# Optimization experiments

Hardware: AMD Instinct MI355X
Metric: run time of the kernel (lower is better)

The kernel has to match this reference:

```python
import jax, jax.numpy as jnp
import numpy as np


def setup_inputs() -> dict:
    key = jax.random.key(0)
    k1, k2 = jax.random.split(key)
    B, S, D, E = 4, 8192, 1024, 64
    x = jax.random.normal(k1, (B, S, D), dtype=jnp.float32)
    W = jax.random.normal(k2, (E, D), dtype=jnp.float32) * (1.0 / np.sqrt(D))
    return {"x": x, "W": W, "top_k": 1}


EXPERT_CAPACITY = 640


def reference(x, W, top_k):
    # Router logits: small-dim linear (bias=False), jitter=0 so no noise.
    logits = jnp.einsum("bsd,ed->bse", x, W)              # [B,S,E]
    probs = jax.nn.softmax(logits, axis=-1)               # [B,S,E]
    num_experts = W.shape[0]
    # top-k over experts (top_k == 1 here)
    top_k_values, top_k_indices = jax.lax.top_k(probs, top_k)  # [B,S,k]
    # one-hot over experts, summed over the k slots -> [B,S,E] int mask
    expert_indices = jax.nn.one_hot(top_k_indices, num_experts, dtype=jnp.int32).sum(axis=-2)
    # token priority: running count of tokens assigned to each expert along seq
    token_priority = jnp.cumsum(expert_indices, axis=-2)  # [B,S,E]
    capacity_mask = token_priority <= EXPERT_CAPACITY
    expert_indices = expert_indices * capacity_mask.astype(jnp.int32)
    # top_k_values [B,S,1] broadcasts over E (valid only for k==1, as in torch)
    router_probs = top_k_values * expert_indices.astype(top_k_values.dtype)
    return expert_indices, router_probs, logits
```

## Files before the change

kernel.cpp:

```cpp
#include <hip/hip_runtime.h>
#include <hip/hip_bf16.h>

#define NB 4
#define NS 8192
#define ND 1024
#define NE 64
#define NM (NB * NS)
#define CAPACITY 640

#define BM 32
#define BK 64
#define NKT (ND / BK)
#define NBLK (NM / BM)
#define C32PB (NS / BM)

#define OCH 64
#define NOB (NM / OCH)

typedef short short8 __attribute__((ext_vector_type(8)));
typedef unsigned short ushort8 __attribute__((ext_vector_type(8)));
typedef float f32x4 __attribute__((ext_vector_type(4)));

__device__ __forceinline__ int swz(int row, int colshorts) {
    return row * 64 + (colshorts ^ ((row & 7) << 3));
}

__global__ __launch_bounds__(256) void w_conv(const float* __restrict__ W,
                                              unsigned short* __restrict__ Wh,
                                              unsigned short* __restrict__ Wl)
{
    const int i = (blockIdx.x * 256 + threadIdx.x) * 4;
    float4 v = *(const float4*)(W + i);
    float f[4] = {v.x, v.y, v.z, v.w};
    ushort4 h, l;
    unsigned short* hp = &h.x;
    unsigned short* lp = &l.x;
#pragma unroll
    for (int c = 0; c < 4; ++c) {
        __hip_bfloat16 hb = __float2bfloat16(f[c]);
        float r = f[c] - __bfloat162float(hb);
        __hip_bfloat16 lb = __float2bfloat16(r);
        hp[c] = __builtin_bit_cast(unsigned short, hb);
        lp[c] = __builtin_bit_cast(unsigned short, lb);
    }
    *(ushort4*)(Wh + i) = h;
    *(ushort4*)(Wl + i) = l;
}

__global__ __launch_bounds__(128) void k1_mfma(const float* __restrict__ x,
                                               const unsigned short* __restrict__ Wh,
                                               const unsigned short* __restrict__ Wl,
                                               float* __restrict__ logits,
                                               int* __restrict__ idx_ws,
                                               float* __restrict__ prob_ws,
                                               int* __restrict__ hist)
{
    __shared__ char sbuf[8192];
    __shared__ short whs[64 * 64];
    __shared__ short wls[64 * 64];
    __shared__ int lh[NE];

    short* xs_h = (short*)sbuf;
    short* xs_l = (short*)(sbuf + 4096);
    float* sLog = (float*)sbuf;

    const int tid = threadIdx.x;
    const int lane = tid & 63;
    const int wv = tid >> 6;
    const int lr = lane & 15;
    const int kq = lane >> 4;
    const int tok0 = blockIdx.x * BM;

    if (tid < NE) lh[tid] = 0;

    const int xrow = tid >> 2;
    const int xcol = (tid & 3) * 16;
    const float* xsrc = x + (size_t)(tok0 + xrow) * ND + xcol;

    const int we0 = tid >> 3;
    const int wcol = (tid & 7) * 8;

    f32x4 acc[4];
#pragma unroll
    for (int j = 0; j < 4; ++j) acc[j] = (f32x4){0.f, 0.f, 0.f, 0.f};

    float4 px[4], px2[4];
#pragma unroll
    for (int c = 0; c < 4; ++c) px[c] = *(const float4*)(xsrc + c * 4);

    for (int kt = 0; kt < NKT; ++kt) {
        const int k0 = kt * BK;
        if (kt > 0) __syncthreads();

#pragma unroll
        for (int i = 0; i < 4; ++i) {
            const int e = we0 + i * 16;
            const size_t gs = (size_t)e * ND + k0 + wcol;
            ushort8 vh = *(const ushort8*)(Wh + gs);
            ushort8 vl = *(const ushort8*)(Wl + gs);
            *(ushort8*)&whs[swz(e, wcol)] = vh;
            *(ushort8*)&wls[swz(e, wcol)] = vl;
        }

#pragma unroll
        for (int c = 0; c < 4; ++c) {
            float f[4] = {px[c].x, px[c].y, px[c].z, px[c].w};
            ushort4 h4, l4;
            unsigned short* hp = &h4.x;
            unsigned short* lp = &l4.x;
#pragma unroll
            for (int e = 0; e < 4; ++e) {
                unsigned int u = __builtin_bit_cast(unsigned int, f[e]);
                hp[e] = (unsigned short)(u >> 16);
                float fhi = __builtin_bit_cast(float, u & 0xFFFF0000u);
                lp[e] = (unsigned short)(__builtin_bit_cast(unsigned int, f[e] - fhi) >> 16);
            }
            const int si = swz(xrow, xcol + c * 4);
            *(ushort4*)&xs_h[si] = h4;
            *(ushort4*)&xs_l[si] = l4;
        }

        if (kt + 1 < NKT) {
#pragma unroll
            for (int c = 0; c < 4; ++c)
                px2[c] = *(const float4*)(xsrc + (k0 + BK) + c * 4);
        }

        __syncthreads();

#pragma unroll
        for (int kk = 0; kk < 2; ++kk) {
            const int col = kk * 32 + kq * 8;
            const int arow = wv * 16 + lr;
            short8 ah = *(const short8*)&xs_h[swz(arow, col)];
            short8 al = *(const short8*)&xs_l[swz(arow, col)];
#pragma unroll
            for (int j = 0; j < 4; ++j) {
                const int erow = j * 16 + lr;
                short8 bh = *(const short8*)&whs[swz(erow, col)];
                short8 bl = *(const short8*)&wls[swz(erow, col)];
                acc[j] = __builtin_amdgcn_mfma_f32_16x16x32_bf16(ah, bh, acc[j], 0, 0, 0);
                acc[j] = __builtin_amdgcn_mfma_f32_16x16x32_bf16(ah, bl, acc[j], 0, 0, 0);
                acc[j] = __builtin_amdgcn_mfma_f32_16x16x32_bf16(al, bh, acc[j], 0, 0, 0);
            }
        }

#pragma unroll
        for (int c = 0; c < 4; ++c) px[c] = px2[c];
    }

    __syncthreads();

#pragma unroll
    for (int r = 0; r < 4; ++r) {
        const int tl = wv * 16 + kq * 4 + r;
        float val[4];
#pragma unroll
        for (int j = 0; j < 4; ++j) val[j] = acc[j][r];

        float m = val[0];
        int mi = lr;
#pragma unroll
        for (int j = 1; j < 4; ++j) {
            if (val[j] > m) { m = val[j]; mi = j * 16 + lr; }
        }
#pragma unroll
        for (int off = 1; off < 16; off <<= 1) {
            float m2 = __shfl_xor(m, off);
            int mi2 = __shfl_xor(mi, off);
            if (m2 > m || (m2 == m && mi2 < mi)) { m = m2; mi = mi2; }
        }
        float s = 0.0f;
#pragma unroll
        for (int j = 0; j < 4; ++j) s += __expf(val[j] - m);
#pragma unroll
        for (int off = 1; off < 16; off <<= 1) s += __shfl_xor(s, off);

#pragma unroll
        for (int j = 0; j < 4; ++j) sLog[tl * NE + j * 16 + lr] = val[j];
        if (lr == 0) {
            idx_ws[tok0 + tl] = mi;
            prob_ws[tok0 + tl] = 1.0f / s;
            atomicAdd(&lh[mi], 1);
        }
    }
    __syncthreads();

    const size_t g0 = (size_t)tok0 * NE;
#pragma unroll
    for (int i = 0; i < 4; ++i) {
        const int fl = i * 512 + tid * 4;
        *(float4*)&logits[g0 + fl] = *(const float4*)&sLog[fl];
    }
    if (tid < NE) hist[blockIdx.x * NE + tid] = lh[tid];
}

__global__ __launch_bounds__(256) void k_out(const int* __restrict__ idx_ws,
                                             const float* __restrict__ prob_ws,
                                             const int* __restrict__ hist,
                                             float* __restrict__ e_out,
                                             float* __restrict__ p_out)
{
    __shared__ int sMi[OCH];
    __shared__ float sPr[OCH];
    __shared__ int sAd[OCH];
    __shared__ int pp[4][NE];

    const int c = blockIdx.x;
    const int b = c >> 7;
    const int s = c & 127;
    const int t0 = c * OCH;
    const int tid = threadIdx.x;
    const int lane = tid & 63;
    const int wv = tid >> 6;

    if (tid < OCH) {
        sMi[tid] = idx_ws[t0 + tid];
        sPr[tid] = prob_ws[t0 + tid];
    }

    {
        int run = 0;
        const int* hrow = hist + (size_t)(b * C32PB) * NE + lane;
        const int n = 2 * s;
        for (int i = wv; i < n; i += 4) run += hrow[i * NE];
        pp[wv][lane] = run;
    }
    __syncthreads();

    if (wv == 0) {
        int run = pp[0][lane] + pp[1][lane] + pp[2][lane] + pp[3][lane];
        for (int j = 0; j < OCH; ++j) {
            if (sMi[j] == lane) { ++run; sAd[j] = (run <= CAPACITY) ? 1 : 0; }
        }
    }
    __syncthreads();

    const size_t g0 = (size_t)t0 * NE;
#pragma unroll
    for (int i = 0; i < 4; ++i) {
        const int fl = i * 1024 + tid * 4;
        const int t = fl >> 6;
        const int e0 = fl & 63;
        const int mi = sMi[t];
        const float pr = sPr[t];
        const int ad = sAd[t];
        float4 ev, pv;
        float* evp = &ev.x;
        float* pvp = &pv.x;
#pragma unroll
        for (int cc = 0; cc < 4; ++cc) {
            const bool hit = (mi == e0 + cc) && ad;
            evp[cc] = hit ? 1.0f : 0.0f;
            pvp[cc] = hit ? pr : 0.0f;
        }
        *(float4*)&e_out[g0 + fl] = ev;
        *(float4*)&p_out[g0 + fl] = pv;
    }
}

extern "C" void kernel_launch(void* const* d_in, const int* in_sizes, int n_in,
                              void* d_out, int out_size, void* d_ws, size_t ws_size,
                              hipStream_t stream)
{
    const float* x = (const float*)d_in[0];
    const float* W = (const float*)d_in[1];

    float* out = (float*)d_out;
    float* e_out = out;
    float* p_out = out + (size_t)NM * NE;
    float* logits = out + 2 * (size_t)NM * NE;

    char* ws = (char*)d_ws;
    int* idx_ws    = (int*)ws;
    float* prob_ws = (float*)(ws + (size_t)NM * 4);
    int* hist      = (int*)(ws + (size_t)NM * 8);
    unsigned short* Wh = (unsigned short*)(ws + (size_t)NM * 8 + (size_t)NBLK * NE * 4);
    unsigned short* Wl = Wh + (size_t)NE * ND;

    w_conv<<<NE * ND / (256 * 4), 256, 0, stream>>>(W, Wh, Wl);
    k1_mfma<<<NBLK, 128, 0, stream>>>(x, Wh, Wl, logits, idx_ws, prob_ws, hist);
    k_out<<<NOB, 256, 0, stream>>>(idx_ws, prob_ws, hist, e_out, p_out);
}
```

Measured before the change: 53.87 us.

## Double-buffer GEMM tiles via direct global-to-LDS loads with 64-token blocks

The router GEMM kernel now moves raw fp32 x and the bf16 W split tiles straight into LDS with global_load_lds, using an XOR swizzle and two buffers so the next K-tile is fetched while the current one feeds the MFMAs. The bf16 hi/lo split of x moves from the staging step to the LDS read path. Blocks grow to 64 tokens and 256 threads, with waves specialised into loaders for x, Wh and Wl. The histogram prefix in k_out is adjusted to the new per-block granularity. This trades register staging and one sync per tile for larger LDS use (64 KB per block), which limits occupancy, and for hand-placed waitcnt and barriers.

```diff
diff --git a/kernel.cpp b/kernel.cpp
--- a/kernel.cpp
+++ b/kernel.cpp
@@ -8,22 +8,22 @@
 #define NM (NB * NS)
 #define CAPACITY 640
 
-#define BM 32
+#define BM 64
 #define BK 64
 #define NKT (ND / BK)
 #define NBLK (NM / BM)
-#define C32PB (NS / BM)
+#define CPB (NS / BM)
 
 #define OCH 64
 #define NOB (NM / OCH)
 
 typedef short short8 __attribute__((ext_vector_type(8)));
-typedef unsigned short ushort8 __attribute__((ext_vector_type(8)));
 typedef float f32x4 __attribute__((ext_vector_type(4)));
 
-__device__ __forceinline__ int swz(int row, int colshorts) {
-    return row * 64 + (colshorts ^ ((row & 7) << 3));
-}
+#define GLOAD16(g, l)                                                          \
+    __builtin_amdgcn_global_load_lds(                                          \
+        (const __attribute__((address_space(1))) void*)(g),                    \
+        (__attribute__((address_space(3))) void*)(l), 16, 0, 0)
 
 __global__ __launch_bounds__(256) void w_conv(const float* __restrict__ W,
                                               unsigned short* __restrict__ Wh,
@@ -47,22 +47,18 @@
     *(ushort4*)(Wl + i) = l;
 }
 
-__global__ __launch_bounds__(128) void k1_mfma(const float* __restrict__ x,
-                                               const unsigned short* __restrict__ Wh,
-                                               const unsigned short* __restrict__ Wl,
-                                               float* __restrict__ logits,
-                                               int* __restrict__ idx_ws,
-                                               float* __restrict__ prob_ws,
-                                               int* __restrict__ hist)
-{
-    __shared__ char sbuf[8192];
-    __shared__ short whs[64 * 64];
-    __shared__ short wls[64 * 64];
+__global__ __launch_bounds__(256, 2) void k1_mfma(const float* __restrict__ x,
+                                                  const unsigned short* __restrict__ Wh,
+                                                  const unsigned short* __restrict__ Wl,
+                                                  float* __restrict__ logits,
+                                                  int* __restrict__ idx_ws,
+                                                  float* __restrict__ prob_ws,
+                                                  int* __restrict__ hist)
+{
+    __shared__ char SL[65536];
     __shared__ int lh[NE];
-
-    short* xs_h = (short*)sbuf;
-    short* xs_l = (short*)(sbuf + 4096);
-    float* sLog = (float*)sbuf;
+    __shared__ int sMi[BM];
+    __shared__ float sPr[BM];
 
     const int tid = threadIdx.x;
     const int lane = tid & 63;
@@ -73,83 +69,91 @@
 
     if (tid < NE) lh[tid] = 0;
 
-    const int xrow = tid >> 2;
-    const int xcol = (tid & 3) * 16;
-    const float* xsrc = x + (size_t)(tok0 + xrow) * ND + xcol;
-
-    const int we0 = tid >> 3;
-    const int wcol = (tid & 7) * 8;
-
     f32x4 acc[4];
 #pragma unroll
     for (int j = 0; j < 4; ++j) acc[j] = (f32x4){0.f, 0.f, 0.f, 0.f};
 
-    float4 px[4], px2[4];
-#pragma unroll
-    for (int c = 0; c < 4; ++c) px[c] = *(const float4*)(xsrc + c * 4);
-
-    for (int kt = 0; kt < NKT; ++kt) {
+    auto stage = [&](int kt, int b) {
         const int k0 = kt * BK;
-        if (kt > 0) __syncthreads();
-
-#pragma unroll
-        for (int i = 0; i < 4; ++i) {
-            const int e = we0 + i * 16;
-            const size_t gs = (size_t)e * ND + k0 + wcol;
-            ushort8 vh = *(const ushort8*)(Wh + gs);
-            ushort8 vl = *(const ushort8*)(Wl + gs);
-            *(ushort8*)&whs[swz(e, wcol)] = vh;
-            *(ushort8*)&wls[swz(e, wcol)] = vl;
-        }
-
-#pragma unroll
-        for (int c = 0; c < 4; ++c) {
-            float f[4] = {px[c].x, px[c].y, px[c].z, px[c].w};
-            ushort4 h4, l4;
-            unsigned short* hp = &h4.x;
-            unsigned short* lp = &l4.x;
-#pragma unroll
-            for (int e = 0; e < 4; ++e) {
-                unsigned int u = __builtin_bit_cast(unsigned int, f[e]);
-                hp[e] = (unsigned short)(u >> 16);
+        if (wv < 2) {
+            const int r0 = wv * 32 + (lane >> 4);
+            const int uslot = lane & 15;
+            char* xd = SL + b * 16384 + wv * 8192;
+#pragma unroll
+            for (int i = 0; i < 8; ++i) {
+                const int r = r0 + i * 4;
+                const int su = uslot ^ (r & 15);
+                const float* g = x + (size_t)(tok0 + r) * ND + k0 + su * 4;
+                GLOAD16(g, xd + i * 1024);
+            }
+        } else {
+            const unsigned short* Ws = (wv == 2) ? Wh : Wl;
+            char* wd = SL + 32768 + (wv - 2) * 16384 + b * 8192;
+            const int r0 = lane >> 3;
+            const int su = (lane & 7) ^ (r0 & 7);
+#pragma unroll
+            for (int i = 0; i < 8; ++i) {
+                const unsigned short* g = Ws + (size_t)(i * 8 + r0) * ND + k0 + su * 8;
+                GLOAD16(g, wd + i * 1024);
+            }
+        }
+    };
+
+    auto compute = [&](int b) {
+        const float* xsb = (const float*)(SL + b * 16384);
+        const short* whb = (const short*)(SL + 32768 + b * 8192);
+        const short* wlb = (const short*)(SL + 49152 + b * 8192);
+        const int arow = wv * 16 + lr;
+        const int xbase = arow * 64;
+#pragma unroll
+        for (int kk = 0; kk < 2; ++kk) {
+            const int su = kk * 8 + kq * 2;
+            f32x4 a0 = *(const f32x4*)&xsb[xbase + ((su)     ^ lr) * 4];
+            f32x4 a1 = *(const f32x4*)&xsb[xbase + ((su + 1) ^ lr) * 4];
+            float f[8] = {a0[0], a0[1], a0[2], a0[3], a1[0], a1[1], a1[2], a1[3]};
+            short8 ah, al;
+#pragma unroll
+            for (int c = 0; c < 8; ++c) {
+                unsigned int u = __builtin_bit_cast(unsigned int, f[c]);
+                ah[c] = (short)(u >> 16);
                 float fhi = __builtin_bit_cast(float, u & 0xFFFF0000u);
-                lp[e] = (unsigned short)(__builtin_bit_cast(unsigned int, f[e] - fhi) >> 16);
-            }
-            const int si = swz(xrow, xcol + c * 4);
-            *(ushort4*)&xs_h[si] = h4;
-            *(ushort4*)&xs_l[si] = l4;
-        }
-
-        if (kt + 1 < NKT) {
-#pragma unroll
-            for (int c = 0; c < 4; ++c)
-                px2[c] = *(const float4*)(xsrc + (k0 + BK) + c * 4);
-        }
-
-        __syncthreads();
-
-#pragma unroll
-        for (int kk = 0; kk < 2; ++kk) {
-            const int col = kk * 32 + kq * 8;
-            const int arow = wv * 16 + lr;
-            short8 ah = *(const short8*)&xs_h[swz(arow, col)];
-            short8 al = *(const short8*)&xs_l[swz(arow, col)];
+                __hip_bfloat16 lb = __float2bfloat16(f[c] - fhi);
+                al[c] = __builtin_bit_cast(short, lb);
+            }
+            const int ucol = kk * 4 + kq;
 #pragma unroll
             for (int j = 0; j < 4; ++j) {
                 const int erow = j * 16 + lr;
-                short8 bh = *(const short8*)&whs[swz(erow, col)];
-                short8 bl = *(const short8*)&wls[swz(erow, col)];
+                const int off = erow * 64 + ((ucol ^ (lr & 7)) * 8);
+                short8 bh = *(const short8*)&whb[off];
+                short8 bl = *(const short8*)&wlb[off];
                 acc[j] = __builtin_amdgcn_mfma_f32_16x16x32_bf16(ah, bh, acc[j], 0, 0, 0);
                 acc[j] = __builtin_amdgcn_mfma_f32_16x16x32_bf16(ah, bl, acc[j], 0, 0, 0);
                 acc[j] = __builtin_amdgcn_mfma_f32_16x16x32_bf16(al, bh, acc[j], 0, 0, 0);
             }
         }
-
-#pragma unroll
-        for (int c = 0; c < 4; ++c) px[c] = px2[c];
-    }
-
-    __syncthreads();
+    };
+
+    stage(0, 0);
+#pragma unroll
+    for (int kt = 0; kt < NKT; ++kt) {
+        const int b = kt & 1;
+        if (kt + 1 < NKT) {
+            stage(kt + 1, b ^ 1);
+            asm volatile("s_waitcnt vmcnt(8)" ::: "memory");
+        } else {
+            asm volatile("s_waitcnt vmcnt(0)" ::: "memory");
+        }
+        __builtin_amdgcn_s_barrier();
+        __builtin_amdgcn_sched_barrier(0);
+        compute(b);
+        __builtin_amdgcn_sched_barrier(0);
+        __builtin_amdgcn_s_barrier();
+    }
+
+    __syncthreads();
+
+    float* sLog = (float*)SL;
 
 #pragma unroll
     for (int r = 0; r < 4; ++r) {
@@ -179,6 +183,7 @@
 #pragma unroll
         for (int j = 0; j < 4; ++j) sLog[tl * NE + j * 16 + lr] = val[j];
         if (lr == 0) {
+            sMi[tl] = mi;
             idx_ws[tok0 + tl] = mi;
             prob_ws[tok0 + tl] = 1.0f / s;
             atomicAdd(&lh[mi], 1);
@@ -189,10 +194,11 @@
     const size_t g0 = (size_t)tok0 * NE;
 #pragma unroll
     for (int i = 0; i < 4; ++i) {
-        const int fl = i * 512 + tid * 4;
+        const int fl = i * 1024 + tid * 4;
         *(float4*)&logits[g0 + fl] = *(const float4*)&sLog[fl];
     }
     if (tid < NE) hist[blockIdx.x * NE + tid] = lh[tid];
+    (void)sMi; (void)sPr;
 }
 
 __global__ __launch_bounds__(256) void k_out(const int* __restrict__ idx_ws,
@@ -221,9 +227,8 @@
 
     {
         int run = 0;
-        const int* hrow = hist + (size_t)(b * C32PB) * NE + lane;
-        const int n = 2 * s;
-        for (int i = wv; i < n; i += 4) run += hrow[i * NE];
+        const int* hrow = hist + (size_t)(b * CPB) * NE + lane;
+        for (int i = wv; i < s; i += 4) run += hrow[i * NE];
         pp[wv][lane] = run;
     }
     __syncthreads();
@@ -279,6 +284,6 @@
     unsigned short* Wl = Wh + (size_t)NE * ND;
 
     w_conv<<<NE * ND / (256 * 4), 256, 0, stream>>>(W, Wh, Wl);
-    k1_mfma<<<NBLK, 128, 0, stream>>>(x, Wh, Wl, logits, idx_ws, prob_ws, hist);
+    k1_mfma<<<NBLK, 256, 0, stream>>>(x, Wh, Wl, logits, idx_ws, prob_ws, hist);
     k_out<<<NOB, 256, 0, stream>>>(idx_ws, prob_ws, hist, e_out, p_out);
 }
```

Result: faster. 47.05 us (-12.6%).
